# Optimization experiments

Measured on AMD Instinct MI355X. Metric: run time of the kernel, lower is better.

The kernel has to match this reference:

```python
import jax, jax.numpy as jnp
import numpy as np

B, S, HID = 2, 2048, 1024
H, HKV, D = 16, 16, 64


def _rope_tables(seq_len, dim, base=10000.0):
    inv_freq = 1.0 / (base ** (np.arange(0, dim, 2, dtype=np.float32) / dim))
    t = np.arange(seq_len, dtype=np.float32)
    freqs = np.outer(t, inv_freq)            # [S, D/2]
    emb = np.concatenate([freqs, freqs], axis=-1)  # [S, D]
    return jnp.asarray(np.cos(emb)), jnp.asarray(np.sin(emb))


def setup_inputs() -> dict:
    key = jax.random.key(0)
    k1, k2, k3 = jax.random.split(key, 3)
    hidden_states = jax.random.normal(k1, (B, S, HID), dtype=jnp.float32)
    cos, sin = _rope_tables(S, D)
    w_qkv = jax.random.normal(k2, ((H + 2 * HKV) * D, HID), dtype=jnp.float32) / np.sqrt(HID)
    w_o = jax.random.normal(k3, (HID, H * D), dtype=jnp.float32) / np.sqrt(H * D)
    return {"hidden_states": hidden_states, "cos": cos, "sin": sin, "w_qkv": w_qkv, "w_o": w_o}


def _rotate_half(x):
    mid = x.shape[-1] // 2
    return jnp.concatenate([-x[..., mid:], x[..., :mid]], axis=-1)


def reference(hidden_states, cos, sin, w_qkv, w_o):
    b, s, _ = hidden_states.shape
    qkv = hidden_states @ w_qkv.T                       # [B,S,(H+2HKV)*D]
    qkv = qkv.reshape(b, s, H + 2 * HKV, D).transpose(0, 2, 1, 3)  # [B,heads,S,D]
    q, k, v = qkv[:, :H], qkv[:, H:H + HKV], qkv[:, H + HKV:]
    # RoPE (cos/sin broadcast [S,D] -> [B,H,S,D])
    q = q * cos + _rotate_half(q) * sin
    k = k * cos + _rotate_half(k) * sin
    # causal SDPA
    scale = 1.0 / jnp.sqrt(jnp.asarray(D, dtype=q.dtype))
    scores = jnp.einsum("bhqd,bhkd->bhqk", q, k) * scale
    causal = jnp.tril(jnp.ones((s, s), dtype=bool))
    scores = jnp.where(causal, scores, jnp.finfo(scores.dtype).min)
    attn = jax.nn.softmax(scores, axis=-1)
    out = jnp.einsum("bhqk,bhkd->bhqd", attn, v)        # [B,H,S,D]
    out = out.transpose(0, 2, 1, 3).reshape(b, s, H * D)
    return out @ w_o.T
```

## Files before the change

kernel.cpp:

```cpp
#include <hip/hip_runtime.h>

typedef __bf16 bf16_t;
typedef __bf16 bf16x8 __attribute__((ext_vector_type(8)));
typedef __bf16 bf16x4 __attribute__((ext_vector_type(4)));
typedef float  f32x4  __attribute__((ext_vector_type(4)));

#define LOG2E 1.44269504088896340736f

__device__ __forceinline__ void gload_lds16(const void* g, void* l) {
  __builtin_amdgcn_global_load_lds(
      (const __attribute__((address_space(1))) void*)g,
      (__attribute__((address_space(3))) void*)l, 16, 0, 0);
}

__device__ __forceinline__ void store_c(float* p, float v)  { *p = v; }
__device__ __forceinline__ void store_c(bf16_t* p, float v) { *p = (bf16_t)v; }

__global__ __launch_bounds__(256) void cast_kernel(const float* __restrict__ in,
                                                   bf16_t* __restrict__ out, int n4) {
  int i = blockIdx.x * 256 + threadIdx.x;
  const int stride = gridDim.x * 256;
  for (; i < n4; i += stride) {
    f32x4 v = *(const f32x4*)(in + (size_t)i * 4);
    bf16x4 o;
#pragma unroll
    for (int j = 0; j < 4; ++j) o[j] = (bf16_t)v[j];
    *(bf16x4*)(out + (size_t)i * 4) = o;
  }
}

template <typename OutT>
__global__ __launch_bounds__(256) void gemm_bt(const bf16_t* __restrict__ A,
                                               const bf16_t* __restrict__ B,
                                               OutT* __restrict__ C,
                                               int M, int N, int K) {
  __shared__ bf16_t As[128 * 32];
  __shared__ bf16_t Bs[128 * 32];
  const int tid  = threadIdx.x;
  const int lane = tid & 63;
  const int wid  = tid >> 6;
  const int wm = wid >> 1, wn = wid & 1;
  const size_t m0 = (size_t)blockIdx.y * 128;
  const size_t n0 = (size_t)blockIdx.x * 128;

  f32x4 acc[4][4] = {};

  for (int k0 = 0; k0 < K; k0 += 32) {
#pragma unroll
    for (int j = 0; j < 2; ++j) {
      const int c = tid + j * 256;
      const int r = c >> 2;
      const int kp = (c & 3) * 8;
      gload_lds16(A + (m0 + r) * K + k0 + kp, As + (size_t)c * 8);
      gload_lds16(B + (n0 + r) * K + k0 + kp, Bs + (size_t)c * 8);
    }
    __syncthreads();

    const int kk = (lane >> 4) * 8;
    const int rs = lane & 15;
    bf16x8 af[4], bfv[4];
#pragma unroll
    for (int t = 0; t < 4; ++t) {
      af[t]  = *(const bf16x8*)(As + (wm * 64 + t * 16 + rs) * 32 + kk);
      bfv[t] = *(const bf16x8*)(Bs + (wn * 64 + t * 16 + rs) * 32 + kk);
    }
#pragma unroll
    for (int mt = 0; mt < 4; ++mt)
#pragma unroll
      for (int nt = 0; nt < 4; ++nt)
        acc[mt][nt] = __builtin_amdgcn_mfma_f32_16x16x32_bf16(af[mt], bfv[nt], acc[mt][nt], 0, 0, 0);
    __syncthreads();
  }

#pragma unroll
  for (int mt = 0; mt < 4; ++mt)
#pragma unroll
    for (int nt = 0; nt < 4; ++nt)
#pragma unroll
      for (int r = 0; r < 4; ++r) {
        size_t row = m0 + wm * 64 + mt * 16 + (lane >> 4) * 4 + r;
        size_t col = n0 + wn * 64 + nt * 16 + (lane & 15);
        store_c(C + row * N + col, acc[mt][nt][r]);
      }
}

__global__ __launch_bounds__(256) void rope_reorg(const bf16_t* __restrict__ qkv,
                                                  const float* __restrict__ cosT,
                                                  const float* __restrict__ sinT,
                                                  bf16_t* __restrict__ Q,
                                                  bf16_t* __restrict__ Kd,
                                                  bf16_t* __restrict__ Vt) {
  __shared__ bf16_t T[64 * 72];
  const int blk  = blockIdx.x;
  const int sblk = blk & 31;
  const int hh   = (blk >> 5) % 48;
  const int b    = blk / (32 * 48);
  const int s0   = sblk * 64;
  const int tid  = threadIdx.x;

  if (hh < 32) {
    const bool isq = hh < 16;
    const int h = isq ? hh : hh - 16;
    bf16_t* dst = (isq ? Q : Kd) + (size_t)(b * 16 + h) * 2048 * 64;
    for (int u = tid; u < 512; u += 256) {
      const int s = u >> 3, oct = u & 7;
      const size_t src = ((size_t)(b * 2048) + s0 + s) * 3072 + hh * 64;
      bf16x8 x = *(const bf16x8*)(qkv + src + oct * 8);
      bf16x8 y = *(const bf16x8*)(qkv + src + ((oct * 8) ^ 32));
      const float* cp = cosT + (size_t)(s0 + s) * 64 + oct * 8;
      const float* sp = sinT + (size_t)(s0 + s) * 64 + oct * 8;
      const float sgn = (oct < 4) ? -1.f : 1.f;
      bf16x8 ov;
#pragma unroll
      for (int j = 0; j < 8; ++j) {
        float xv = (float)x[j], yv = (float)y[j];
        ov[j] = (bf16_t)(xv * cp[j] + sgn * yv * sp[j]);
      }
      *(bf16x8*)(dst + (size_t)(s0 + s) * 64 + oct * 8) = ov;
    }
  } else {
    const int hv = hh - 32;
    for (int u = tid; u < 512; u += 256) {
      const int s = u >> 3, oct = u & 7;
      *(bf16x8*)(&T[s * 72 + oct * 8]) =
          *(const bf16x8*)(qkv + ((size_t)(b * 2048) + s0 + s) * 3072 + hh * 64 + oct * 8);
    }
    __syncthreads();
    bf16_t* dst = Vt + (size_t)(b * 16 + hv) * 64 * 2048;
    for (int u = tid; u < 512; u += 256) {
      const int d = u >> 3, soct = u & 7;
      bf16x8 w;
#pragma unroll
      for (int j = 0; j < 8; ++j) w[j] = T[(soct * 8 + j) * 72 + d];
      *(bf16x8*)(dst + (size_t)d * 2048 + s0 + soct * 8) = w;
    }
  }
}

__global__ __launch_bounds__(256) void attn_kernel(const bf16_t* __restrict__ Q,
                                                   const bf16_t* __restrict__ Kt,
                                                   const bf16_t* __restrict__ Vt,
                                                   bf16_t* __restrict__ O) {
  const int bid  = blockIdx.x;
  const int xcd  = bid & 7;
  const int idx  = bid >> 3;
  const int bh   = xcd * 4 + (idx & 3);
  const int qblk = 31 - (idx >> 2);
  const int b    = bh >> 4;
  const int h    = bh & 15;
  const int tid  = threadIdx.x;
  const int lane = tid & 63;
  const int wid  = tid >> 6;
  const bf16_t* Qb = Q  + (size_t)bh * 2048 * 64;
  const bf16_t* Kb = Kt + (size_t)bh * 2048 * 64;
  const bf16_t* Vb = Vt + (size_t)bh * 64 * 2048;

  __shared__ bf16_t Ps[4][16 * 72];

  const int q0  = qblk * 64 + wid * 16;
  const int l15 = lane & 15;
  const int g   = lane >> 4;
  const int dd  = g * 8;
  const int qmax = q0 + 15;
  const int ntiles = qmax / 64 + 1;
  const float SC = 0.125f * LOG2E;

  bf16x8 qf0 = *(const bf16x8*)(Qb + (size_t)(q0 + l15) * 64 + dd);
  bf16x8 qf1 = *(const bf16x8*)(Qb + (size_t)(q0 + l15) * 64 + 32 + dd);

  f32x4 o[4] = {};
  float mr[4], lr[4];
#pragma unroll
  for (int r = 0; r < 4; ++r) { mr[r] = -3.0e38f; lr[r] = 0.f; }

  auto prefK = [&](int tt, bf16x8 (&kf)[4][2]) {
    if (tt >= ntiles) return;
    const int kv0 = tt * 64;
#pragma unroll
    for (int kt = 0; kt < 4; ++kt) {
      const bf16_t* kp = Kb + (size_t)(kv0 + kt * 16 + l15) * 64;
      kf[kt][0] = *(const bf16x8*)(kp + dd);
      kf[kt][1] = *(const bf16x8*)(kp + 32 + dd);
    }
  };
  auto prefV = [&](int tt, bf16x8 (&vf)[2][4]) {
    if (tt >= ntiles) return;
    const int kv0 = tt * 64;
#pragma unroll
    for (int half = 0; half < 2; ++half)
#pragma unroll
      for (int dt = 0; dt < 4; ++dt)
        vf[half][dt] = *(const bf16x8*)(Vb + (size_t)(dt * 16 + l15) * 2048 + kv0 + half * 32 + dd);
  };

  auto compute = [&](bf16x8 (&kf)[4][2], bf16x8 (&vf)[2][4], int kv0) {
    f32x4 st[4];
#pragma unroll
    for (int kt = 0; kt < 4; ++kt) {
      f32x4 acc = {};
      acc = __builtin_amdgcn_mfma_f32_16x16x32_bf16(qf0, kf[kt][0], acc, 0, 0, 0);
      acc = __builtin_amdgcn_mfma_f32_16x16x32_bf16(qf1, kf[kt][1], acc, 0, 0, 0);
      st[kt] = acc;
    }

    if (kv0 + 63 > q0) {
#pragma unroll
      for (int kt = 0; kt < 4; ++kt)
#pragma unroll
        for (int r = 0; r < 4; ++r) {
          const int kg = kv0 + kt * 16 + l15;
          const int qg = q0 + g * 4 + r;
          if (kg > qg) st[kt][r] = -3.0e38f;
        }
    }

    float p[4][4];
    float al[4];
#pragma unroll
    for (int r = 0; r < 4; ++r) {
      float mb = fmaxf(fmaxf(st[0][r], st[1][r]), fmaxf(st[2][r], st[3][r]));
      mb = fmaxf(mb, __shfl_xor(mb, 1));
      mb = fmaxf(mb, __shfl_xor(mb, 2));
      mb = fmaxf(mb, __shfl_xor(mb, 4));
      mb = fmaxf(mb, __shfl_xor(mb, 8));
      const float mn = fmaxf(mr[r], mb);
      al[r] = __builtin_amdgcn_exp2f((mr[r] - mn) * SC);
      const float mc = mn * SC;
      float lb = 0.f;
#pragma unroll
      for (int kt = 0; kt < 4; ++kt) {
        p[kt][r] = __builtin_amdgcn_exp2f(__builtin_fmaf(st[kt][r], SC, -mc));
        lb += p[kt][r];
      }
      lb += __shfl_xor(lb, 1);
      lb += __shfl_xor(lb, 2);
      lb += __shfl_xor(lb, 4);
      lb += __shfl_xor(lb, 8);
      lr[r] = lr[r] * al[r] + lb;
      mr[r] = mn;
    }
#pragma unroll
    for (int dt = 0; dt < 4; ++dt)
#pragma unroll
      for (int r = 0; r < 4; ++r) o[dt][r] *= al[r];

#pragma unroll
    for (int kt = 0; kt < 4; ++kt)
#pragma unroll
      for (int r = 0; r < 4; ++r)
        Ps[wid][(g * 4 + r) * 72 + kt * 16 + l15] = (bf16_t)p[kt][r];

    asm volatile("s_waitcnt lgkmcnt(0)" ::: "memory");
    __builtin_amdgcn_sched_barrier(0);

#pragma unroll
    for (int half = 0; half < 2; ++half) {
      if (kv0 + half * 32 > qmax) break;
      bf16x8 pa = *(const bf16x8*)(&Ps[wid][l15 * 72 + half * 32 + dd]);
#pragma unroll
      for (int dt = 0; dt < 4; ++dt)
        o[dt] = __builtin_amdgcn_mfma_f32_16x16x32_bf16(pa, vf[half][dt], o[dt], 0, 0, 0);
    }
  };

  bf16x8 ka[4][2], kb2[4][2], vcur[2][4];
  prefK(0, ka);
  for (int t = 0; t < ntiles; t += 2) {
    prefK(t + 1, kb2);
    prefV(t, vcur);
    compute(ka, vcur, t * 64);
    prefK(t + 2, ka);
    prefV(t + 1, vcur);
    if (t + 1 < ntiles) compute(kb2, vcur, (t + 1) * 64);
  }

#pragma unroll
  for (int r = 0; r < 4; ++r) {
    const float inv = 1.f / lr[r];
    size_t srow = (size_t)b * 2048 + q0 + g * 4 + r;
#pragma unroll
    for (int dt = 0; dt < 4; ++dt)
      O[srow * 1024 + h * 64 + dt * 16 + l15] = (bf16_t)(o[dt][r] * inv);
  }
}

extern "C" void kernel_launch(void* const* d_in, const int* in_sizes, int n_in,
                              void* d_out, int out_size, void* d_ws, size_t ws_size,
                              hipStream_t stream) {
  const float* hs   = (const float*)d_in[0];
  const float* cosT = (const float*)d_in[1];
  const float* sinT = (const float*)d_in[2];
  const float* wqkv = (const float*)d_in[3];
  const float* wo   = (const float*)d_in[4];
  float* out = (float*)d_out;

  char* ws = (char*)d_ws;
  bf16_t* hs_b   = (bf16_t*)(ws);
  bf16_t* wqkv_b = (bf16_t*)(ws + 8388608);
  bf16_t* wo_b   = (bf16_t*)(ws + 14680064);
  bf16_t* qkv    = (bf16_t*)(ws + 16777216);
  bf16_t* Qb     = (bf16_t*)(ws + 41943040);
  bf16_t* Kb     = (bf16_t*)(ws + 50331648);
  bf16_t* Vtb    = (bf16_t*)(ws + 58720256);
  bf16_t* aout   = (bf16_t*)(ws + 67108864);

  cast_kernel<<<2048, 256, 0, stream>>>(hs,   hs_b,   4194304 / 4);
  cast_kernel<<<1024, 256, 0, stream>>>(wqkv, wqkv_b, 3145728 / 4);
  cast_kernel<<<512,  256, 0, stream>>>(wo,   wo_b,   1048576 / 4);

  gemm_bt<bf16_t><<<dim3(24, 32), 256, 0, stream>>>(hs_b, wqkv_b, qkv, 4096, 3072, 1024);

  rope_reorg<<<3072, 256, 0, stream>>>(qkv, cosT, sinT, Qb, Kb, Vtb);

  attn_kernel<<<1024, 256, 0, stream>>>(Qb, Kb, Vtb, aout);

  gemm_bt<float><<<dim3(8, 32), 256, 0, stream>>>(aout, wo_b, out, 4096, 1024, 1024);
}
```

Baseline: 276.9 us.

## Compute transposed scores to keep P in registers and drop LDS round-trip

The attention kernel now computes S^T = K·Q^T by swapping the MFMA operands, so each lane holds one query column. The softmax row max and sum then reduce across only two shuffles instead of four, and the probabilities can be packed directly into the B operand of the PV MFMA. This removes the shared-memory store/load of P and its waitcnt barrier. V is loaded as two 4-element halves and joined so its layout matches the permuted k ordering, and the output is written as vectorized bf16x4 stores. The risks are narrower V loads and extra register pressure from the split V fragments.

```diff
diff --git a/kernel.cpp b/kernel.cpp
--- a/kernel.cpp
+++ b/kernel.cpp
@@ -4,6 +4,9 @@
 typedef __bf16 bf16x8 __attribute__((ext_vector_type(8)));
 typedef __bf16 bf16x4 __attribute__((ext_vector_type(4)));
 typedef float  f32x4  __attribute__((ext_vector_type(4)));
+typedef unsigned int u32;
+typedef u32 u32x2 __attribute__((ext_vector_type(2)));
+typedef u32 u32x4 __attribute__((ext_vector_type(4)));
 
 #define LOG2E 1.44269504088896340736f
 
@@ -155,23 +158,21 @@
   const bf16_t* Kb = Kt + (size_t)bh * 2048 * 64;
   const bf16_t* Vb = Vt + (size_t)bh * 64 * 2048;
 
-  __shared__ bf16_t Ps[4][16 * 72];
-
   const int q0  = qblk * 64 + wid * 16;
   const int l15 = lane & 15;
   const int g   = lane >> 4;
+  const int g4  = g * 4;
   const int dd  = g * 8;
+  const int qg  = q0 + l15;
   const int qmax = q0 + 15;
-  const int ntiles = qmax / 64 + 1;
+  const int ntiles = qblk + 1;
   const float SC = 0.125f * LOG2E;
 
-  bf16x8 qf0 = *(const bf16x8*)(Qb + (size_t)(q0 + l15) * 64 + dd);
-  bf16x8 qf1 = *(const bf16x8*)(Qb + (size_t)(q0 + l15) * 64 + 32 + dd);
+  bf16x8 qf0 = *(const bf16x8*)(Qb + (size_t)qg * 64 + dd);
+  bf16x8 qf1 = *(const bf16x8*)(Qb + (size_t)qg * 64 + 32 + dd);
 
   f32x4 o[4] = {};
-  float mr[4], lr[4];
-#pragma unroll
-  for (int r = 0; r < 4; ++r) { mr[r] = -3.0e38f; lr[r] = 0.f; }
+  float m_run = -3.0e38f, l_run = 0.f;
 
   auto prefK = [&](int tt, bf16x8 (&kf)[4][2]) {
     if (tt >= ntiles) return;
@@ -183,23 +184,34 @@
       kf[kt][1] = *(const bf16x8*)(kp + 32 + dd);
     }
   };
-  auto prefV = [&](int tt, bf16x8 (&vf)[2][4]) {
+  auto prefV = [&](int tt, bf16x4 (&vl)[2][4], bf16x4 (&vh)[2][4]) {
     if (tt >= ntiles) return;
     const int kv0 = tt * 64;
 #pragma unroll
-    for (int half = 0; half < 2; ++half)
-#pragma unroll
-      for (int dt = 0; dt < 4; ++dt)
-        vf[half][dt] = *(const bf16x8*)(Vb + (size_t)(dt * 16 + l15) * 2048 + kv0 + half * 32 + dd);
+    for (int c = 0; c < 2; ++c)
+#pragma unroll
+      for (int dt = 0; dt < 4; ++dt) {
+        const bf16_t* vp = Vb + (size_t)(dt * 16 + l15) * 2048 + kv0 + 32 * c + g4;
+        vl[c][dt] = *(const bf16x4*)(vp);
+        vh[c][dt] = *(const bf16x4*)(vp + 16);
+      }
   };
 
-  auto compute = [&](bf16x8 (&kf)[4][2], bf16x8 (&vf)[2][4], int kv0) {
+  auto join = [](bf16x4 lo, bf16x4 hi2) -> bf16x8 {
+    u32x2 a = __builtin_bit_cast(u32x2, lo);
+    u32x2 c = __builtin_bit_cast(u32x2, hi2);
+    u32x4 w = {a[0], a[1], c[0], c[1]};
+    return __builtin_bit_cast(bf16x8, w);
+  };
+
+  auto compute = [&](bf16x8 (&kf)[4][2], bf16x4 (&vl)[2][4], bf16x4 (&vh)[2][4],
+                     int kv0) {
     f32x4 st[4];
 #pragma unroll
     for (int kt = 0; kt < 4; ++kt) {
       f32x4 acc = {};
-      acc = __builtin_amdgcn_mfma_f32_16x16x32_bf16(qf0, kf[kt][0], acc, 0, 0, 0);
-      acc = __builtin_amdgcn_mfma_f32_16x16x32_bf16(qf1, kf[kt][1], acc, 0, 0, 0);
+      acc = __builtin_amdgcn_mfma_f32_16x16x32_bf16(kf[kt][0], qf0, acc, 0, 0, 0);
+      acc = __builtin_amdgcn_mfma_f32_16x16x32_bf16(kf[kt][1], qf1, acc, 0, 0, 0);
       st[kt] = acc;
     }
 
@@ -208,79 +220,83 @@
       for (int kt = 0; kt < 4; ++kt)
 #pragma unroll
         for (int r = 0; r < 4; ++r) {
-          const int kg = kv0 + kt * 16 + l15;
-          const int qg = q0 + g * 4 + r;
-          if (kg > qg) st[kt][r] = -3.0e38f;
+          const int kg = kv0 + kt * 16 + g4 + r;
+          st[kt][r] = (kg > qg) ? -1.0e30f : st[kt][r];
         }
     }
 
+    float mb = -3.0e38f;
+#pragma unroll
+    for (int kt = 0; kt < 4; ++kt) {
+      float a = fmaxf(st[kt][0], st[kt][1]);
+      float bm = fmaxf(st[kt][2], st[kt][3]);
+      mb = fmaxf(mb, fmaxf(a, bm));
+    }
+    mb = fmaxf(mb, __shfl_xor(mb, 16));
+    mb = fmaxf(mb, __shfl_xor(mb, 32));
+
+    const float mn = fmaxf(m_run, mb);
+    const float al = __builtin_amdgcn_exp2f((m_run - mn) * SC);
+    m_run = mn;
+    const float mc = mn * SC;
+
     float p[4][4];
-    float al[4];
-#pragma unroll
-    for (int r = 0; r < 4; ++r) {
-      float mb = fmaxf(fmaxf(st[0][r], st[1][r]), fmaxf(st[2][r], st[3][r]));
-      mb = fmaxf(mb, __shfl_xor(mb, 1));
-      mb = fmaxf(mb, __shfl_xor(mb, 2));
-      mb = fmaxf(mb, __shfl_xor(mb, 4));
-      mb = fmaxf(mb, __shfl_xor(mb, 8));
-      const float mn = fmaxf(mr[r], mb);
-      al[r] = __builtin_amdgcn_exp2f((mr[r] - mn) * SC);
-      const float mc = mn * SC;
-      float lb = 0.f;
-#pragma unroll
-      for (int kt = 0; kt < 4; ++kt) {
+    float lb = 0.f;
+#pragma unroll
+    for (int kt = 0; kt < 4; ++kt)
+#pragma unroll
+      for (int r = 0; r < 4; ++r) {
         p[kt][r] = __builtin_amdgcn_exp2f(__builtin_fmaf(st[kt][r], SC, -mc));
         lb += p[kt][r];
       }
-      lb += __shfl_xor(lb, 1);
-      lb += __shfl_xor(lb, 2);
-      lb += __shfl_xor(lb, 4);
-      lb += __shfl_xor(lb, 8);
-      lr[r] = lr[r] * al[r] + lb;
-      mr[r] = mn;
-    }
+    lb += __shfl_xor(lb, 16);
+    lb += __shfl_xor(lb, 32);
+    l_run = l_run * al + lb;
+
 #pragma unroll
     for (int dt = 0; dt < 4; ++dt)
 #pragma unroll
-      for (int r = 0; r < 4; ++r) o[dt][r] *= al[r];
-
-#pragma unroll
-    for (int kt = 0; kt < 4; ++kt)
-#pragma unroll
-      for (int r = 0; r < 4; ++r)
-        Ps[wid][(g * 4 + r) * 72 + kt * 16 + l15] = (bf16_t)p[kt][r];
-
-    asm volatile("s_waitcnt lgkmcnt(0)" ::: "memory");
-    __builtin_amdgcn_sched_barrier(0);
-
-#pragma unroll
-    for (int half = 0; half < 2; ++half) {
-      if (kv0 + half * 32 > qmax) break;
-      bf16x8 pa = *(const bf16x8*)(&Ps[wid][l15 * 72 + half * 32 + dd]);
+      for (int r = 0; r < 4; ++r) o[dt][r] *= al;
+
+    bf16x8 pf0, pf1;
+#pragma unroll
+    for (int j = 0; j < 4; ++j) {
+      pf0[j]     = (bf16_t)p[0][j];
+      pf0[j + 4] = (bf16_t)p[1][j];
+      pf1[j]     = (bf16_t)p[2][j];
+      pf1[j + 4] = (bf16_t)p[3][j];
+    }
+
+#pragma unroll
+    for (int dt = 0; dt < 4; ++dt)
+      o[dt] = __builtin_amdgcn_mfma_f32_16x16x32_bf16(join(vl[0][dt], vh[0][dt]), pf0, o[dt], 0, 0, 0);
+    if (kv0 + 32 <= qmax) {
 #pragma unroll
       for (int dt = 0; dt < 4; ++dt)
-        o[dt] = __builtin_amdgcn_mfma_f32_16x16x32_bf16(pa, vf[half][dt], o[dt], 0, 0, 0);
+        o[dt] = __builtin_amdgcn_mfma_f32_16x16x32_bf16(join(vl[1][dt], vh[1][dt]), pf1, o[dt], 0, 0, 0);
     }
   };
 
-  bf16x8 ka[4][2], kb2[4][2], vcur[2][4];
+  bf16x8 ka[4][2], kb2[4][2];
+  bf16x4 vcl[2][4], vch[2][4];
   prefK(0, ka);
   for (int t = 0; t < ntiles; t += 2) {
     prefK(t + 1, kb2);
-    prefV(t, vcur);
-    compute(ka, vcur, t * 64);
+    prefV(t, vcl, vch);
+    compute(ka, vcl, vch, t * 64);
     prefK(t + 2, ka);
-    prefV(t + 1, vcur);
-    if (t + 1 < ntiles) compute(kb2, vcur, (t + 1) * 64);
-  }
-
-#pragma unroll
-  for (int r = 0; r < 4; ++r) {
-    const float inv = 1.f / lr[r];
-    size_t srow = (size_t)b * 2048 + q0 + g * 4 + r;
-#pragma unroll
-    for (int dt = 0; dt < 4; ++dt)
-      O[srow * 1024 + h * 64 + dt * 16 + l15] = (bf16_t)(o[dt][r] * inv);
+    prefV(t + 1, vcl, vch);
+    if (t + 1 < ntiles) compute(kb2, vcl, vch, (t + 1) * 64);
+  }
+
+  const float inv = 1.f / l_run;
+  bf16_t* Ob = O + ((size_t)(b * 2048) + qg) * 1024 + h * 64;
+#pragma unroll
+  for (int dt = 0; dt < 4; ++dt) {
+    bf16x4 w;
+#pragma unroll
+    for (int r = 0; r < 4; ++r) w[r] = (bf16_t)(o[dt][r] * inv);
+    *(bf16x4*)(Ob + dt * 16 + g4) = w;
   }
 }
 
```

New measurement: 343.2 us. 23.9% more time.
